# Performance work log

Measured on AMD Instinct MI355X. Metric: run time of the kernel, lower is better.

Reference implementation:

```python
import jax, jax.numpy as jnp
import numpy as np

IN_DIM = 1024
HID = 1024
BATCH = 4096


def _linear_params(key, out_dim, in_dim):
    # torch nn.Linear default init: U(-1/sqrt(in_dim), 1/sqrt(in_dim))
    kw, kb = jax.random.split(key)
    bound = 1.0 / np.sqrt(in_dim)
    W = jax.random.uniform(kw, (out_dim, in_dim), jnp.float32, -bound, bound)
    b = jax.random.uniform(kb, (out_dim,), jnp.float32, -bound, bound)
    return W, b


def setup_inputs() -> dict:
    key = jax.random.key(0)
    keys = jax.random.split(key, 11)
    x = jax.random.normal(keys[0], (BATCH, IN_DIM), jnp.float32)
    h_1 = jax.random.normal(keys[1], (BATCH, HID), jnp.float32)
    c_1 = jax.random.normal(keys[2], (BATCH, HID), jnp.float32)
    names = ['ix', 'ih', 'fx', 'fh', 'ox', 'oh', 'cx', 'ch']
    inp = {'x': x, 'h_1': h_1, 'c_1': c_1}
    for i, n in enumerate(names):
        in_d = IN_DIM if n[1] == 'x' else HID
        W, b = _linear_params(keys[3 + i], HID, in_d)
        inp[f'W_{n}'] = W
        inp[f'b_{n}'] = b
    return inp


def reference(x, h_1, c_1,
              W_ix, b_ix, W_ih, b_ih,
              W_fx, b_fx, W_fh, b_fh,
              W_ox, b_ox, W_oh, b_oh,
              W_cx, b_cx, W_ch, b_ch):
    # Fuse the 8 small GEMMs into two big ones: [B,in]x[in,4H] and [B,H]x[H,4H]
    Wx = jnp.concatenate([W_ix, W_fx, W_ox, W_cx], axis=0)  # [4H, in]
    Wh = jnp.concatenate([W_ih, W_fh, W_oh, W_ch], axis=0)  # [4H, H]
    bx = jnp.concatenate([b_ix, b_fx, b_ox, b_cx])          # [4H]
    bh = jnp.concatenate([b_ih, b_fh, b_oh, b_ch])          # [4H]
    gates = x @ Wx.T + h_1 @ Wh.T + (bx + bh)               # [B, 4H]
    gi, gf, go, gc = jnp.split(gates, 4, axis=-1)
    i = jax.nn.sigmoid(gi)
    f = jax.nn.sigmoid(gf)
    o = jax.nn.sigmoid(go)
    c_ = jnp.tanh(gc)
    c = f * c_1 + i * c_
    h = o * jnp.tanh(c)
    return (h, c)
```

## Files before the change

kernel.cpp:

```cpp
#include <hip/hip_runtime.h>


typedef __attribute__((ext_vector_type(4))) float  f32x4;
typedef __attribute__((ext_vector_type(8))) __bf16 bf16x8;
typedef __attribute__((ext_vector_type(8))) short  s16x8;

#define HID    1024
#define BATCH  4096
#define KDIM   2048
#define PANEL_STRIDE (128 * KDIM)
#define KT_STRIDE    4096

__device__ __forceinline__ unsigned short f2bf(float f) {
  unsigned u = __builtin_bit_cast(unsigned, f);
  u += 0x7FFFu + ((u >> 16) & 1u);
  return (unsigned short)(u >> 16);
}
__device__ __forceinline__ float bf2f(unsigned short s) {
  return __builtin_bit_cast(float, (unsigned)s << 16);
}

__global__ void convert_kernel(
    const float* __restrict__ x,   const float* __restrict__ h,
    const float* __restrict__ Wix, const float* __restrict__ Wfx,
    const float* __restrict__ Wox, const float* __restrict__ Wcx,
    const float* __restrict__ Wih, const float* __restrict__ Wfh,
    const float* __restrict__ Woh, const float* __restrict__ Wch,
    const float* __restrict__ bix, const float* __restrict__ bfx,
    const float* __restrict__ box, const float* __restrict__ bcx,
    const float* __restrict__ bih, const float* __restrict__ bfh,
    const float* __restrict__ boh, const float* __restrict__ bch,
    short* __restrict__ Ahi, short* __restrict__ Bhi, short* __restrict__ Blo,
    float* __restrict__ bias)
{
  const int bid = blockIdx.x;
  const int t   = threadIdx.x;
  const int r   = t >> 1;
  const int kh  = t & 1;
  const bool isA = bid < 2048;
  const int pb = isA ? bid : (bid - 2048);
  const int p  = pb >> 6;
  const int kt = pb & 63;
  const int kk = kt * 32 + kh * 16;

  const float* srow;
  if (isA) {
    const int m = p * 128 + r;
    srow = (kk < 1024) ? (x + (size_t)m * 1024 + kk)
                       : (h + (size_t)m * 1024 + (kk - 1024));
  } else {
    const int np = p * 128 + r;
    const int j = ((np >> 6) << 4) + (np & 15);
    const int gate = (np >> 4) & 3;
    const float* wx = (gate == 0) ? Wix : (gate == 1) ? Wfx : (gate == 2) ? Wox : Wcx;
    const float* wh = (gate == 0) ? Wih : (gate == 1) ? Wfh : (gate == 2) ? Woh : Wch;
    srow = (kk < 1024) ? (wx + (size_t)j * 1024 + kk)
                       : (wh + (size_t)j * 1024 + (kk - 1024));
    if (kt == 0 && t < 128) {
      const int np2 = p * 128 + t;
      const int j2 = ((np2 >> 6) << 4) + (np2 & 15);
      const int g2 = (np2 >> 4) & 3;
      const float* bx  = (g2 == 0) ? bix : (g2 == 1) ? bfx : (g2 == 2) ? box : bcx;
      const float* bh2 = (g2 == 0) ? bih : (g2 == 1) ? bfh : (g2 == 2) ? boh : bch;
      bias[np2] = bx[j2] + bh2[j2];
    }
  }
  f32x4 v0 = ((const f32x4*)srow)[0];
  f32x4 v1 = ((const f32x4*)srow)[1];
  f32x4 v2 = ((const f32x4*)srow)[2];
  f32x4 v3 = ((const f32x4*)srow)[3];
  s16x8 h0, l0, h1, l1;
  #pragma unroll
  for (int c = 0; c < 8; ++c) {
    float f0 = (c < 4) ? v0[c & 3] : v1[c & 3];
    unsigned short a = f2bf(f0);
    h0[c] = (short)a; l0[c] = (short)f2bf(f0 - bf2f(a));
    float f1 = (c < 4) ? v2[c & 3] : v3[c & 3];
    unsigned short b = f2bf(f1);
    h1[c] = (short)b; l1[c] = (short)f2bf(f1 - bf2f(b));
  }
  const size_t base = ((size_t)p * 64 + kt) * KT_STRIDE + (size_t)(kh * 2) * 1024 + (size_t)r * 8;
  if (isA) {
    *(s16x8*)(Ahi + base) = h0; *(s16x8*)(Ahi + base + 1024) = h1;
  } else {
    *(s16x8*)(Bhi + base) = h0; *(s16x8*)(Bhi + base + 1024) = h1;
    *(s16x8*)(Blo + base) = l0; *(s16x8*)(Blo + base + 1024) = l1;
  }
}

#define GLD16(SRC, DST) \
  __builtin_amdgcn_global_load_lds((const __attribute__((address_space(1))) void*)(SRC), \
                                   (__attribute__((address_space(3))) void*)(DST), 16, 0, 0)

__device__ __forceinline__ float sigmoid_f(float v) { return 1.f / (1.f + __expf(-v)); }
__device__ __forceinline__ float tanh_f(float v) {
  float t = __expf(-2.f * fabsf(v));
  float r = (1.f - t) / (1.f + t);
  return copysignf(r, v);
}

__global__ __launch_bounds__(256, 3) void gemm_fused_kernel(
    const short* __restrict__ Ahi,
    const short* __restrict__ Bhi, const short* __restrict__ Blo,
    const float* __restrict__ bias, const float* __restrict__ c1,
    float* __restrict__ out)
{
  __shared__ __align__(16) short sA[2 * 3 * 4096];

  const int tid = threadIdx.x, wave = tid >> 6, lane = tid & 63;
  int bid = blockIdx.x;
  bid = (bid & 7) * 128 + (bid >> 3);
  const int by = bid >> 5, bx = bid & 31;
  const int m0 = by * 128, n0 = bx * 128;
  const int wr = (wave >> 1) * 64, wc = (wave & 1) * 64;

  const short* pAh = Ahi + (size_t)by * PANEL_STRIDE;
  const short* pBh = Bhi + (size_t)bx * PANEL_STRIDE;
  const short* pBl = Blo + (size_t)bx * PANEL_STRIDE;

  f32x4 acc[4][4];
  #pragma unroll
  for (int i = 0; i < 4; ++i)
    #pragma unroll
    for (int j = 0; j < 4; ++j)
      acc[i][j] = (f32x4){0.f, 0.f, 0.f, 0.f};

  const int c0   = wave * 2;
  const int loff = lane * 8;

  #define STAGE(BUF, KT) do {                                            \
    const size_t koff = (size_t)(KT) * KT_STRIDE;                        \
    const int sb_ = (BUF) * 12288;                                       \
    _Pragma("unroll")                                                    \
    for (int i_ = 0; i_ < 2; ++i_) {                                     \
      const int c_ = c0 + i_;                                            \
      GLD16(pAh + koff + c_ * 512 + loff, &sA[sb_ + c_ * 512]);          \
      GLD16(pBh + koff + c_ * 512 + loff, &sA[sb_ + 4096 + c_ * 512]);   \
      GLD16(pBl + koff + c_ * 512 + loff, &sA[sb_ + 8192 + c_ * 512]);   \
    }                                                                    \
  } while (0)

  STAGE(0, 0);
  __syncthreads();

  const int g = lane >> 4, frow = lane & 15;
  for (int kt = 0; kt < 64; ++kt) {
    const int cur = kt & 1;
    if (kt < 63) STAGE(cur ^ 1, kt + 1);
    const int sb = cur * 12288;
    bf16x8 ah[4], bh[4], bl[4];
    #pragma unroll
    for (int f = 0; f < 4; ++f) {
      const int ra = g * 1024 + (wr + f * 16 + frow) * 8;
      ah[f] = *(const bf16x8*)&sA[sb + ra];
      const int rb = g * 1024 + (wc + f * 16 + frow) * 8;
      bh[f] = *(const bf16x8*)&sA[sb + 4096 + rb];
      bl[f] = *(const bf16x8*)&sA[sb + 8192 + rb];
    }
    #pragma unroll
    for (int fm = 0; fm < 4; ++fm)
      #pragma unroll
      for (int fn = 0; fn < 4; ++fn) {
        acc[fm][fn] = __builtin_amdgcn_mfma_f32_16x16x32_bf16(ah[fm], bh[fn], acc[fm][fn], 0, 0, 0);
        acc[fm][fn] = __builtin_amdgcn_mfma_f32_16x16x32_bf16(ah[fm], bl[fn], acc[fm][fn], 0, 0, 0);
      }
    __syncthreads();
  }

  const int l15 = lane & 15;
  const int j   = (bx * 32) + ((wc >> 6) << 4) + l15;
  const float bv0 = bias[n0 + wc +  0 + l15];
  const float bv1 = bias[n0 + wc + 16 + l15];
  const float bv2 = bias[n0 + wc + 32 + l15];
  const float bv3 = bias[n0 + wc + 48 + l15];
  const int row0 = m0 + wr + ((lane >> 4) << 2);
  #pragma unroll
  for (int fm = 0; fm < 4; ++fm)
    #pragma unroll
    for (int rr = 0; rr < 4; ++rr) {
      const int m = row0 + fm * 16 + rr;
      const float I  = sigmoid_f(acc[fm][0][rr] + bv0);
      const float F  = sigmoid_f(acc[fm][1][rr] + bv1);
      const float O  = sigmoid_f(acc[fm][2][rr] + bv2);
      const float Ct = tanh_f(acc[fm][3][rr] + bv3);
      const float cc = F * c1[(size_t)m * HID + j] + I * Ct;
      out[(size_t)m * HID + j]                       = O * tanh_f(cc);
      out[(size_t)BATCH * HID + (size_t)m * HID + j] = cc;
    }
  #undef STAGE
}

extern "C" void kernel_launch(void* const* d_in, const int* in_sizes, int n_in,
                              void* d_out, int out_size, void* d_ws, size_t ws_size,
                              hipStream_t stream) {
  const float* x    = (const float*)d_in[0];
  const float* h1   = (const float*)d_in[1];
  const float* c1   = (const float*)d_in[2];
  const float* W_ix = (const float*)d_in[3];  const float* b_ix = (const float*)d_in[4];
  const float* W_ih = (const float*)d_in[5];  const float* b_ih = (const float*)d_in[6];
  const float* W_fx = (const float*)d_in[7];  const float* b_fx = (const float*)d_in[8];
  const float* W_fh = (const float*)d_in[9];  const float* b_fh = (const float*)d_in[10];
  const float* W_ox = (const float*)d_in[11]; const float* b_ox = (const float*)d_in[12];
  const float* W_oh = (const float*)d_in[13]; const float* b_oh = (const float*)d_in[14];
  const float* W_cx = (const float*)d_in[15]; const float* b_cx = (const float*)d_in[16];
  const float* W_ch = (const float*)d_in[17]; const float* b_ch = (const float*)d_in[18];

  short* Ahi = (short*)d_ws;
  short* Bhi = Ahi + (size_t)8 * 1024 * 1024;
  short* Blo = Bhi + (size_t)8 * 1024 * 1024;
  float* bias = (float*)(Blo + (size_t)8 * 1024 * 1024);

  convert_kernel<<<4096, 256, 0, stream>>>(x, h1,
      W_ix, W_fx, W_ox, W_cx, W_ih, W_fh, W_oh, W_ch,
      b_ix, b_fx, b_ox, b_cx, b_ih, b_fh, b_oh, b_ch,
      Ahi, Bhi, Blo, bias);

  gemm_fused_kernel<<<1024, 256, 0, stream>>>(Ahi, Bhi, Blo, bias, c1, (float*)d_out);
}
```

Before: 298.3 us.

## Enlarge GEMM tile to 256x256 with 8 waves and triple-buffered LDS pipeline

The fused LSTM GEMM moves from 128x128 tiles with 4 waves and double buffering to 256x256 tiles with 8 waves, a 3-stage LDS ring, and loads issued two k-steps ahead. Staging is split into sub-chunks interleaved with four MFMA quadrants, separated by barriers and s_setprio. The goal is more operand reuse per LDS byte and better overlap of global-to-LDS copies with MFMA work. In exchange the grid shrinks to 256 blocks, about one per CU, and each wave holds 128 accumulator registers, so occupancy is lower and the extra barriers can cost time.

```diff
diff --git a/kernel.cpp b/kernel.cpp
--- a/kernel.cpp
+++ b/kernel.cpp
@@ -8,8 +8,7 @@
 #define HID    1024
 #define BATCH  4096
 #define KDIM   2048
-#define PANEL_STRIDE (128 * KDIM)
-#define KT_STRIDE    4096
+#define KT_STRIDE 4096
 
 __device__ __forceinline__ unsigned short f2bf(float f) {
   unsigned u = __builtin_bit_cast(unsigned, f);
@@ -99,83 +98,116 @@
   return copysignf(r, v);
 }
 
-__global__ __launch_bounds__(256, 3) void gemm_fused_kernel(
+__global__ __launch_bounds__(512, 2) void gemm_fused_kernel(
     const short* __restrict__ Ahi,
     const short* __restrict__ Bhi, const short* __restrict__ Blo,
     const float* __restrict__ bias, const float* __restrict__ c1,
     float* __restrict__ out)
 {
-  __shared__ __align__(16) short sA[2 * 3 * 4096];
+  __shared__ __align__(16) short sA[3 * 24576];
 
   const int tid = threadIdx.x, wave = tid >> 6, lane = tid & 63;
   int bid = blockIdx.x;
-  bid = (bid & 7) * 128 + (bid >> 3);
-  const int by = bid >> 5, bx = bid & 31;
-  const int m0 = by * 128, n0 = bx * 128;
-  const int wr = (wave >> 1) * 64, wc = (wave & 1) * 64;
-
-  const short* pAh = Ahi + (size_t)by * PANEL_STRIDE;
-  const short* pBh = Bhi + (size_t)bx * PANEL_STRIDE;
-  const short* pBl = Blo + (size_t)bx * PANEL_STRIDE;
-
-  f32x4 acc[4][4];
-  #pragma unroll
-  for (int i = 0; i < 4; ++i)
-    #pragma unroll
-    for (int j = 0; j < 4; ++j)
-      acc[i][j] = (f32x4){0.f, 0.f, 0.f, 0.f};
-
-  const int c0   = wave * 2;
+  bid = (bid & 7) * 32 + (bid >> 3);
+  const int by = bid >> 4, bx = bid & 15;
+  const int wm = wave >> 2, wn = wave & 3;
+  const int g = lane >> 4, frow = lane & 15;
   const int loff = lane * 8;
 
-  #define STAGE(BUF, KT) do {                                            \
-    const size_t koff = (size_t)(KT) * KT_STRIDE;                        \
-    const int sb_ = (BUF) * 12288;                                       \
-    _Pragma("unroll")                                                    \
-    for (int i_ = 0; i_ < 2; ++i_) {                                     \
-      const int c_ = c0 + i_;                                            \
-      GLD16(pAh + koff + c_ * 512 + loff, &sA[sb_ + c_ * 512]);          \
-      GLD16(pBh + koff + c_ * 512 + loff, &sA[sb_ + 4096 + c_ * 512]);   \
-      GLD16(pBl + koff + c_ * 512 + loff, &sA[sb_ + 8192 + c_ * 512]);   \
-    }                                                                    \
+  f32x4 acc[8][4];
+  #pragma unroll
+  for (int i = 0; i < 8; ++i)
+    #pragma unroll
+    for (int j = 0; j < 4; ++j) acc[i][j] = (f32x4){0.f, 0.f, 0.f, 0.f};
+
+#define STAGE1(I_, KT2, SBUF) do {                                                      \
+    const int idx_ = wave * 6 + (I_);                                                   \
+    const int pl_ = idx_ >> 4, c_ = (idx_ >> 3) & 1, s_ = idx_ & 7;                     \
+    const short* gsrc_; int ldst_;                                                      \
+    if (pl_ == 0)      { gsrc_ = Ahi + (size_t)((2*by + c_) * 64 + (KT2)) * KT_STRIDE;  \
+                         ldst_ = (SBUF) + c_ * 4096; }                                  \
+    else if (pl_ == 1) { gsrc_ = Bhi + (size_t)((2*bx + c_) * 64 + (KT2)) * KT_STRIDE;  \
+                         ldst_ = (SBUF) + 8192 + c_ * 4096; }                           \
+    else               { gsrc_ = Blo + (size_t)((2*bx + c_) * 64 + (KT2)) * KT_STRIDE;  \
+                         ldst_ = (SBUF) + 16384 + c_ * 4096; }                          \
+    GLD16(gsrc_ + s_ * 512 + loff, &sA[ldst_ + s_ * 512]);                              \
   } while (0)
 
-  STAGE(0, 0);
-  __syncthreads();
-
-  const int g = lane >> 4, frow = lane & 15;
+#define MFMA_Q(FM0, FN0)                                                                 \
+    _Pragma("unroll")                                                                    \
+    for (int f_ = 0; f_ < 4; ++f_) {                                                     \
+      acc[(FM0)+f_][(FN0)  ] = __builtin_amdgcn_mfma_f32_16x16x32_bf16(ah[f_], bh[0], acc[(FM0)+f_][(FN0)  ], 0, 0, 0); \
+      acc[(FM0)+f_][(FN0)  ] = __builtin_amdgcn_mfma_f32_16x16x32_bf16(ah[f_], bl[0], acc[(FM0)+f_][(FN0)  ], 0, 0, 0); \
+      acc[(FM0)+f_][(FN0)+1] = __builtin_amdgcn_mfma_f32_16x16x32_bf16(ah[f_], bh[1], acc[(FM0)+f_][(FN0)+1], 0, 0, 0); \
+      acc[(FM0)+f_][(FN0)+1] = __builtin_amdgcn_mfma_f32_16x16x32_bf16(ah[f_], bl[1], acc[(FM0)+f_][(FN0)+1], 0, 0, 0); \
+    }
+
+  #pragma unroll
+  for (int i = 0; i < 6; ++i) STAGE1(i, 0, 0);
+  #pragma unroll
+  for (int i = 0; i < 6; ++i) STAGE1(i, 1, 24576);
+
   for (int kt = 0; kt < 64; ++kt) {
-    const int cur = kt & 1;
-    if (kt < 63) STAGE(cur ^ 1, kt + 1);
-    const int sb = cur * 12288;
-    bf16x8 ah[4], bh[4], bl[4];
-    #pragma unroll
-    for (int f = 0; f < 4; ++f) {
-      const int ra = g * 1024 + (wr + f * 16 + frow) * 8;
-      ah[f] = *(const bf16x8*)&sA[sb + ra];
-      const int rb = g * 1024 + (wc + f * 16 + frow) * 8;
-      bh[f] = *(const bf16x8*)&sA[sb + 4096 + rb];
-      bl[f] = *(const bf16x8*)&sA[sb + 8192 + rb];
-    }
-    #pragma unroll
-    for (int fm = 0; fm < 4; ++fm)
-      #pragma unroll
-      for (int fn = 0; fn < 4; ++fn) {
-        acc[fm][fn] = __builtin_amdgcn_mfma_f32_16x16x32_bf16(ah[fm], bh[fn], acc[fm][fn], 0, 0, 0);
-        acc[fm][fn] = __builtin_amdgcn_mfma_f32_16x16x32_bf16(ah[fm], bl[fn], acc[fm][fn], 0, 0, 0);
-      }
-    __syncthreads();
-  }
-
-  const int l15 = lane & 15;
-  const int j   = (bx * 32) + ((wc >> 6) << 4) + l15;
-  const float bv0 = bias[n0 + wc +  0 + l15];
-  const float bv1 = bias[n0 + wc + 16 + l15];
-  const float bv2 = bias[n0 + wc + 32 + l15];
-  const float bv3 = bias[n0 + wc + 48 + l15];
-  const int row0 = m0 + wr + ((lane >> 4) << 2);
-  #pragma unroll
-  for (int fm = 0; fm < 4; ++fm)
+    if (kt < 62) asm volatile("s_waitcnt vmcnt(6)" ::: "memory");
+    else         asm volatile("s_waitcnt vmcnt(0)" ::: "memory");
+    __builtin_amdgcn_s_barrier();
+
+    const int sb  = (kt % 3) * 24576;
+    const int sb2 = ((kt + 2) % 3) * 24576;
+    const bool st = (kt < 62);
+    const int abase  = sb + wm * 4096 + g * 1024 + frow * 8;
+    const int bboff  = (wn >> 1) * 4096 + g * 1024 + ((wn & 1) * 64 + frow) * 8;
+    const int bhbase = sb + 8192  + bboff;
+    const int blbase = sb + 16384 + bboff;
+
+    bf16x8 ah[4], bh[2], bl[2];
+
+    #pragma unroll
+    for (int f_ = 0; f_ < 4; ++f_) ah[f_] = *(const bf16x8*)&sA[abase + f_ * 128];
+    bh[0] = *(const bf16x8*)&sA[bhbase];       bh[1] = *(const bf16x8*)&sA[bhbase + 128];
+    bl[0] = *(const bf16x8*)&sA[blbase];       bl[1] = *(const bf16x8*)&sA[blbase + 128];
+    if (st) { STAGE1(0, kt + 2, sb2); STAGE1(1, kt + 2, sb2); }
+    __builtin_amdgcn_s_barrier();
+    __builtin_amdgcn_s_setprio(1);
+    MFMA_Q(0, 0)
+    __builtin_amdgcn_s_setprio(0);
+    __builtin_amdgcn_s_barrier();
+
+    bh[0] = *(const bf16x8*)&sA[bhbase + 256]; bh[1] = *(const bf16x8*)&sA[bhbase + 384];
+    bl[0] = *(const bf16x8*)&sA[blbase + 256]; bl[1] = *(const bf16x8*)&sA[blbase + 384];
+    if (st) { STAGE1(2, kt + 2, sb2); STAGE1(3, kt + 2, sb2); }
+    __builtin_amdgcn_s_barrier();
+    __builtin_amdgcn_s_setprio(1);
+    MFMA_Q(0, 2)
+    __builtin_amdgcn_s_setprio(0);
+    __builtin_amdgcn_s_barrier();
+
+    #pragma unroll
+    for (int f_ = 0; f_ < 4; ++f_) ah[f_] = *(const bf16x8*)&sA[abase + 512 + f_ * 128];
+    if (st) { STAGE1(4, kt + 2, sb2); STAGE1(5, kt + 2, sb2); }
+    __builtin_amdgcn_s_barrier();
+    __builtin_amdgcn_s_setprio(1);
+    MFMA_Q(4, 2)
+    __builtin_amdgcn_s_setprio(0);
+    __builtin_amdgcn_s_barrier();
+
+    bh[0] = *(const bf16x8*)&sA[bhbase];       bh[1] = *(const bf16x8*)&sA[bhbase + 128];
+    bl[0] = *(const bf16x8*)&sA[blbase];       bl[1] = *(const bf16x8*)&sA[blbase + 128];
+    __builtin_amdgcn_s_barrier();
+    __builtin_amdgcn_s_setprio(1);
+    MFMA_Q(4, 0)
+    __builtin_amdgcn_s_setprio(0);
+  }
+
+  const int n0 = bx * 256;
+  const int j  = bx * 64 + wn * 16 + frow;
+  const float bv0 = bias[n0 + wn * 64 +  0 + frow];
+  const float bv1 = bias[n0 + wn * 64 + 16 + frow];
+  const float bv2 = bias[n0 + wn * 64 + 32 + frow];
+  const float bv3 = bias[n0 + wn * 64 + 48 + frow];
+  const int row0 = by * 256 + wm * 128 + g * 4;
+  #pragma unroll
+  for (int fm = 0; fm < 8; ++fm)
     #pragma unroll
     for (int rr = 0; rr < 4; ++rr) {
       const int m = row0 + fm * 16 + rr;
@@ -187,7 +219,8 @@
       out[(size_t)m * HID + j]                       = O * tanh_f(cc);
       out[(size_t)BATCH * HID + (size_t)m * HID + j] = cc;
     }
-  #undef STAGE
+  #undef STAGE1
+  #undef MFMA_Q
 }
 
 extern "C" void kernel_launch(void* const* d_in, const int* in_sizes, int n_in,
@@ -215,5 +248,5 @@
       b_ix, b_fx, b_ox, b_cx, b_ih, b_fh, b_oh, b_ch,
       Ahi, Bhi, Blo, bias);
 
-  gemm_fused_kernel<<<1024, 256, 0, stream>>>(Ahi, Bhi, Blo, bias, c1, (float*)d_out);
-}
+  gemm_fused_kernel<<<256, 512, 0, stream>>>(Ahi, Bhi, Blo, bias, c1, (float*)d_out);
+}
```

New measurement: 280.3 us. 6.0% less time.

## Use 256x256 tiles, 32x32 MFMA and triple-buffered LDS pipeline in fused LSTM GEMM

Applied to the files above, without the earlier changes.

Enlarges the output tile from 128x128 to 256x256 with 8 waves per block and moves from 16x16x32 to 32x32x16 bf16 MFMA. It reorders the gate layout (i,o,f,c) so the epilogue can pair gates via a lane shuffle. The main loop uses a three-stage LDS ring with explicit vmcnt waits, split barriers and setprio around MFMA bursts. The aim is less global/LDS traffic per FLOP and better overlap of loads with compute. The costs are 256 blocks on 256 CUs (a single wave with no tail slack), higher register and LDS pressure, and a more complex hand-written schedule.

```diff
diff --git a/kernel.cpp b/kernel.cpp
--- a/kernel.cpp
+++ b/kernel.cpp
@@ -1,9 +1,10 @@
 #include <hip/hip_runtime.h>
 
 
-typedef __attribute__((ext_vector_type(4))) float  f32x4;
-typedef __attribute__((ext_vector_type(8))) __bf16 bf16x8;
-typedef __attribute__((ext_vector_type(8))) short  s16x8;
+typedef __attribute__((ext_vector_type(4)))  float  f32x4;
+typedef __attribute__((ext_vector_type(16))) float  f32x16;
+typedef __attribute__((ext_vector_type(8)))  __bf16 bf16x8;
+typedef __attribute__((ext_vector_type(8)))  short  s16x8;
 
 #define HID    1024
 #define BATCH  4096
@@ -51,17 +52,17 @@
   } else {
     const int np = p * 128 + r;
     const int j = ((np >> 6) << 4) + (np & 15);
-    const int gate = (np >> 4) & 3;
-    const float* wx = (gate == 0) ? Wix : (gate == 1) ? Wfx : (gate == 2) ? Wox : Wcx;
-    const float* wh = (gate == 0) ? Wih : (gate == 1) ? Wfh : (gate == 2) ? Woh : Wch;
+    const int pos = (np >> 4) & 3;
+    const float* wx = (pos == 0) ? Wix : (pos == 1) ? Wox : (pos == 2) ? Wfx : Wcx;
+    const float* wh = (pos == 0) ? Wih : (pos == 1) ? Woh : (pos == 2) ? Wfh : Wch;
     srow = (kk < 1024) ? (wx + (size_t)j * 1024 + kk)
                        : (wh + (size_t)j * 1024 + (kk - 1024));
     if (kt == 0 && t < 128) {
       const int np2 = p * 128 + t;
       const int j2 = ((np2 >> 6) << 4) + (np2 & 15);
-      const int g2 = (np2 >> 4) & 3;
-      const float* bx  = (g2 == 0) ? bix : (g2 == 1) ? bfx : (g2 == 2) ? box : bcx;
-      const float* bh2 = (g2 == 0) ? bih : (g2 == 1) ? bfh : (g2 == 2) ? boh : bch;
+      const int p2 = (np2 >> 4) & 3;
+      const float* bx  = (p2 == 0) ? bix : (p2 == 1) ? box : (p2 == 2) ? bfx : bcx;
+      const float* bh2 = (p2 == 0) ? bih : (p2 == 1) ? boh : (p2 == 2) ? bfh : bch;
       bias[np2] = bx[j2] + bh2[j2];
     }
   }
@@ -99,95 +100,143 @@
   return copysignf(r, v);
 }
 
-__global__ __launch_bounds__(256, 3) void gemm_fused_kernel(
+__global__ __launch_bounds__(512, 2) void gemm_fused_kernel(
     const short* __restrict__ Ahi,
     const short* __restrict__ Bhi, const short* __restrict__ Blo,
     const float* __restrict__ bias, const float* __restrict__ c1,
     float* __restrict__ out)
 {
-  __shared__ __align__(16) short sA[2 * 3 * 4096];
+  __shared__ __align__(16) short sA[3 * 24576];
 
   const int tid = threadIdx.x, wave = tid >> 6, lane = tid & 63;
   int bid = blockIdx.x;
-  bid = (bid & 7) * 128 + (bid >> 3);
-  const int by = bid >> 5, bx = bid & 31;
-  const int m0 = by * 128, n0 = bx * 128;
-  const int wr = (wave >> 1) * 64, wc = (wave & 1) * 64;
-
-  const short* pAh = Ahi + (size_t)by * PANEL_STRIDE;
-  const short* pBh = Bhi + (size_t)bx * PANEL_STRIDE;
-  const short* pBl = Blo + (size_t)bx * PANEL_STRIDE;
-
-  f32x4 acc[4][4];
+  bid = (bid & 7) * 32 + (bid >> 3);
+  const int by = bid >> 4, bx = bid & 15;
+  const int wm = wave >> 2, wn = wave & 3;
+  const int l31 = lane & 31, lhi = lane >> 5;
+  const int loff = lane * 8;
+
+  f32x16 acc[4][2];
   #pragma unroll
   for (int i = 0; i < 4; ++i)
     #pragma unroll
-    for (int j = 0; j < 4; ++j)
-      acc[i][j] = (f32x4){0.f, 0.f, 0.f, 0.f};
-
-  const int c0   = wave * 2;
-  const int loff = lane * 8;
-
-  #define STAGE(BUF, KT) do {                                            \
-    const size_t koff = (size_t)(KT) * KT_STRIDE;                        \
-    const int sb_ = (BUF) * 12288;                                       \
-    _Pragma("unroll")                                                    \
-    for (int i_ = 0; i_ < 2; ++i_) {                                     \
-      const int c_ = c0 + i_;                                            \
-      GLD16(pAh + koff + c_ * 512 + loff, &sA[sb_ + c_ * 512]);          \
-      GLD16(pBh + koff + c_ * 512 + loff, &sA[sb_ + 4096 + c_ * 512]);   \
-      GLD16(pBl + koff + c_ * 512 + loff, &sA[sb_ + 8192 + c_ * 512]);   \
-    }                                                                    \
-  } while (0)
-
-  STAGE(0, 0);
-  __syncthreads();
-
-  const int g = lane >> 4, frow = lane & 15;
-  for (int kt = 0; kt < 64; ++kt) {
-    const int cur = kt & 1;
-    if (kt < 63) STAGE(cur ^ 1, kt + 1);
-    const int sb = cur * 12288;
-    bf16x8 ah[4], bh[4], bl[4];
+    for (int j = 0; j < 2; ++j)
+      #pragma unroll
+      for (int r = 0; r < 16; ++r) acc[i][j][r] = 0.f;
+
+#define MKQ(Q, D, IDX) {                                                     \
+    const int pl_ = (IDX) >> 4, ch_ = ((IDX) >> 3) & 1, ss_ = (IDX) & 7;     \
+    const short* pb_ = (pl_ == 0) ? (Ahi + (size_t)(2*by + ch_) * PANEL_STRIDE) \
+                     : (pl_ == 1) ? (Bhi + (size_t)(2*bx + ch_) * PANEL_STRIDE) \
+                                  : (Blo + (size_t)(2*bx + ch_) * PANEL_STRIDE); \
+    Q = pb_ + ss_ * 512 + loff;                                              \
+    D = pl_ * 8192 + ch_ * 4096 + ss_ * 512; }
+
+  const short *q0, *q1, *q2, *q3, *q4, *q5;
+  int d0, d1, d2, d3, d4, d5;
+  const int ix0 = wave * 6;
+  MKQ(q0, d0, ix0)     MKQ(q1, d1, ix0 + 1) MKQ(q2, d2, ix0 + 2)
+  MKQ(q3, d3, ix0 + 3) MKQ(q4, d4, ix0 + 4) MKQ(q5, d5, ix0 + 5)
+
+#define STG(Q, D, KT2, SB2) GLD16((Q) + (size_t)(KT2) * KT_STRIDE, &sA[(SB2) + (D)])
+
+#define BODY(SB, SB2, KT2, VMN, DS) {                                         \
+    asm volatile("s_waitcnt vmcnt(" #VMN ")" ::: "memory");                   \
+    __builtin_amdgcn_s_barrier();                                             \
+    bf16x8 av[2][2], bfr[2][2][2];                                            \
+    _Pragma("unroll") for (int kh = 0; kh < 2; ++kh) {                        \
+      const int g2o = (SB) + (2*kh + lhi) * 1024;                             \
+      _Pragma("unroll") for (int tm = 0; tm < 2; ++tm)                        \
+        av[tm][kh] = *(const bf16x8*)&sA[g2o + wm*4096 + (tm*32 + l31)*8];    \
+      _Pragma("unroll") for (int tn = 0; tn < 2; ++tn) {                      \
+        const int bo_ = g2o + (wn>>1)*4096 + ((wn&1)*64 + tn*32 + l31)*8;     \
+        bfr[tn][kh][0] = *(const bf16x8*)&sA[bo_ + 8192];                     \
+        bfr[tn][kh][1] = *(const bf16x8*)&sA[bo_ + 16384];                    \
+      }                                                                       \
+    }                                                                         \
+    if (DS) { STG(q0,d0,KT2,SB2); STG(q1,d1,KT2,SB2); STG(q2,d2,KT2,SB2); }   \
+    __builtin_amdgcn_s_barrier();                                             \
+    __builtin_amdgcn_s_setprio(1);                                            \
+    _Pragma("unroll") for (int kh = 0; kh < 2; ++kh)                          \
+      _Pragma("unroll") for (int tm = 0; tm < 2; ++tm)                        \
+        _Pragma("unroll") for (int tn = 0; tn < 2; ++tn)                      \
+          acc[tm][tn] = __builtin_amdgcn_mfma_f32_32x32x16_bf16(              \
+              av[tm][kh], bfr[tn][kh][0], acc[tm][tn], 0, 0, 0);              \
+    _Pragma("unroll") for (int kh = 0; kh < 2; ++kh)                          \
+      _Pragma("unroll") for (int tm = 0; tm < 2; ++tm)                        \
+        _Pragma("unroll") for (int tn = 0; tn < 2; ++tn)                      \
+          acc[tm][tn] = __builtin_amdgcn_mfma_f32_32x32x16_bf16(              \
+              av[tm][kh], bfr[tn][kh][1], acc[tm][tn], 0, 0, 0);              \
+    __builtin_amdgcn_s_setprio(0);                                            \
+    __builtin_amdgcn_s_barrier();                                             \
+    _Pragma("unroll") for (int kh = 0; kh < 2; ++kh) {                        \
+      const int g2o = (SB) + (2*kh + lhi) * 1024;                             \
+      _Pragma("unroll") for (int tm = 0; tm < 2; ++tm)                        \
+        av[tm][kh] = *(const bf16x8*)&sA[g2o + wm*4096 + ((tm+2)*32 + l31)*8];\
+    }                                                                         \
+    if (DS) { STG(q3,d3,KT2,SB2); STG(q4,d4,KT2,SB2); STG(q5,d5,KT2,SB2); }   \
+    __builtin_amdgcn_s_barrier();                                             \
+    __builtin_amdgcn_s_setprio(1);                                            \
+    _Pragma("unroll") for (int kh = 0; kh < 2; ++kh)                          \
+      _Pragma("unroll") for (int tm = 0; tm < 2; ++tm)                        \
+        _Pragma("unroll") for (int tn = 0; tn < 2; ++tn)                      \
+          acc[tm+2][tn] = __builtin_amdgcn_mfma_f32_32x32x16_bf16(            \
+              av[tm][kh], bfr[tn][kh][0], acc[tm+2][tn], 0, 0, 0);            \
+    _Pragma("unroll") for (int kh = 0; kh < 2; ++kh)                          \
+      _Pragma("unroll") for (int tm = 0; tm < 2; ++tm)                        \
+        _Pragma("unroll") for (int tn = 0; tn < 2; ++tn)                      \
+          acc[tm+2][tn] = __builtin_amdgcn_mfma_f32_32x32x16_bf16(            \
+              av[tm][kh], bfr[tn][kh][1], acc[tm+2][tn], 0, 0, 0);            \
+    __builtin_amdgcn_s_setprio(0);                                            \
+  }
+
+  STG(q0,d0,0,0); STG(q1,d1,0,0); STG(q2,d2,0,0);
+  STG(q3,d3,0,0); STG(q4,d4,0,0); STG(q5,d5,0,0);
+  STG(q0,d0,1,24576); STG(q1,d1,1,24576); STG(q2,d2,1,24576);
+  STG(q3,d3,1,24576); STG(q4,d4,1,24576); STG(q5,d5,1,24576);
+
+  for (int t3 = 0; t3 < 60; t3 += 3) {
+    BODY(0,     49152, t3 + 2, 6, true)
+    BODY(24576, 0,     t3 + 3, 6, true)
+    BODY(49152, 24576, t3 + 4, 6, true)
+  }
+  BODY(0,     49152, 62, 6, true)
+  BODY(24576, 0,     63, 6, true)
+  BODY(49152, 0, 0, 6, false)
+  BODY(0,     0, 0, 0, false)
+
+  const int jj = l31 & 15;
+  const int n0 = bx * 256 + wn * 64;
+  const int j  = bx * 64 + wn * 16 + jj;
+  const float b_i = bias[n0 + jj];
+  const float b_o = bias[n0 + 16 + jj];
+  const float b_f = bias[n0 + 32 + jj];
+  const float b_c = bias[n0 + 48 + jj];
+  const bool lo = (l31 < 16);
+  const int rbase = by * 256 + wm * 128 + 4 * lhi;
+  #pragma unroll
+  for (int tm = 0; tm < 4; ++tm)
     #pragma unroll
-    for (int f = 0; f < 4; ++f) {
-      const int ra = g * 1024 + (wr + f * 16 + frow) * 8;
-      ah[f] = *(const bf16x8*)&sA[sb + ra];
-      const int rb = g * 1024 + (wc + f * 16 + frow) * 8;
-      bh[f] = *(const bf16x8*)&sA[sb + 4096 + rb];
-      bl[f] = *(const bf16x8*)&sA[sb + 8192 + rb];
+    for (int r = 0; r < 16; ++r) {
+      const int m = rbase + tm * 32 + (r & 3) + 8 * (r >> 2);
+      const float V0 = acc[tm][0][r], V1 = acc[tm][1][r];
+      const float p0 = __shfl_xor(V0, 16);
+      const float p1 = __shfl_xor(V1, 16);
+      const float gi = lo ? V0 : p0, gf = lo ? V1 : p1;
+      const float go = lo ? p0 : V0, gc = lo ? p1 : V1;
+      const float I  = sigmoid_f(gi + b_i);
+      const float F  = sigmoid_f(gf + b_f);
+      const float O  = sigmoid_f(go + b_o);
+      const float Ct = tanh_f(gc + b_c);
+      const float cc = F * c1[(size_t)m * HID + j] + I * Ct;
+      if (lo) {
+        out[(size_t)m * HID + j]                       = O * tanh_f(cc);
+        out[(size_t)BATCH * HID + (size_t)m * HID + j] = cc;
+      }
     }
-    #pragma unroll
-    for (int fm = 0; fm < 4; ++fm)
-      #pragma unroll
-      for (int fn = 0; fn < 4; ++fn) {
-        acc[fm][fn] = __builtin_amdgcn_mfma_f32_16x16x32_bf16(ah[fm], bh[fn], acc[fm][fn], 0, 0, 0);
-        acc[fm][fn] = __builtin_amdgcn_mfma_f32_16x16x32_bf16(ah[fm], bl[fn], acc[fm][fn], 0, 0, 0);
-      }
-    __syncthreads();
-  }
-
-  const int l15 = lane & 15;
-  const int j   = (bx * 32) + ((wc >> 6) << 4) + l15;
-  const float bv0 = bias[n0 + wc +  0 + l15];
-  const float bv1 = bias[n0 + wc + 16 + l15];
-  const float bv2 = bias[n0 + wc + 32 + l15];
-  const float bv3 = bias[n0 + wc + 48 + l15];
-  const int row0 = m0 + wr + ((lane >> 4) << 2);
-  #pragma unroll
-  for (int fm = 0; fm < 4; ++fm)
-    #pragma unroll
-    for (int rr = 0; rr < 4; ++rr) {
-      const int m = row0 + fm * 16 + rr;
-      const float I  = sigmoid_f(acc[fm][0][rr] + bv0);
-      const float F  = sigmoid_f(acc[fm][1][rr] + bv1);
-      const float O  = sigmoid_f(acc[fm][2][rr] + bv2);
-      const float Ct = tanh_f(acc[fm][3][rr] + bv3);
-      const float cc = F * c1[(size_t)m * HID + j] + I * Ct;
-      out[(size_t)m * HID + j]                       = O * tanh_f(cc);
-      out[(size_t)BATCH * HID + (size_t)m * HID + j] = cc;
-    }
-  #undef STAGE
+  #undef BODY
+  #undef STG
+  #undef MKQ
 }
 
 extern "C" void kernel_launch(void* const* d_in, const int* in_sizes, int n_in,
@@ -215,5 +264,5 @@
       b_ix, b_fx, b_ox, b_cx, b_ih, b_fh, b_oh, b_ch,
       Ahi, Bhi, Blo, bias);
 
-  gemm_fused_kernel<<<1024, 256, 0, stream>>>(Ahi, Bhi, Blo, bias, c1, (float*)d_out);
-}
+  gemm_fused_kernel<<<256, 512, 0, stream>>>(Ahi, Bhi, Blo, bias, c1, (float*)d_out);
+}
```

Measured after the change: 306.2 us. 2.7% more time.
